# Performance work log

Measured on AMD Instinct MI355X. Metric: run time of the kernel, lower is better.

## Reference

```python
import jax, jax.numpy as jnp
import numpy as np

OSF = 15.0  # over_sample_factor
EXPMAX = 50.0
AFROMZERO = 0.02
AFROMC = 0.01


def zmax_calc(a, b, c=1.0):
    # a is a scalar, b (= b*mT^2) is per-element, c == 1.0
    a_is_zero = a < AFROMZERO
    a_is_c = jnp.abs(a - c) < AFROMC
    z_zero = jnp.where(c > b, b / c, 1.0)
    z_c = b / (b + c)
    denom = jnp.where(a_is_c, 1.0, c - a)  # safe denom; branch masked below
    z_gen = 0.5 * (b + c - jnp.sqrt((b - c) ** 2 + 4.0 * a * b)) / denom
    z_gen = jnp.where((z_gen > 0.9999) & (b > 100.0), jnp.minimum(z_gen, 1.0 - a / b), z_gen)
    return jnp.where(a_is_zero, z_zero, jnp.where(a_is_c, z_c, z_gen))


def likelihood(z, mT, a, b):
    # Lund fragmentation f(z) ratio kernel, c = 1.0
    b_exp = b * mT ** 2
    z_max = zmax_calc(a, b_exp, 1.0)
    f_exp = b_exp * (1.0 / z_max - 1.0 / z) + jnp.log(z_max / z)
    a_coef = a * jnp.log((1.0 - z) / (1.0 - z_max))
    f_exp = f_exp + jnp.where(a < AFROMZERO, 0.0, a_coef)
    return jnp.exp(jnp.clip(f_exp, -EXPMAX, EXPMAX))


def setup_inputs() -> dict:
    key = jax.random.key(0)
    kz, kr, km, kmult, kdrop, kzero = jax.random.split(key, 6)
    B, M, R = 8192, 128, 24  # batch, max multiplicity, reject slots
    mult = jax.random.randint(kmult, (B,), 20, M + 1)  # event multiplicities
    valid = jnp.arange(M)[None, :] < mult[:, None]  # [B, M]

    z_acc = jax.random.uniform(kz, (B, M), minval=0.05, maxval=0.95)
    z_acc = jnp.where(valid & (jax.random.uniform(kzero, (B, M)) > 0.1), z_acc, 0.0)

    z_rej = jax.random.uniform(kr, (B, M, R), minval=0.05, maxval=0.95)
    keep = jax.random.uniform(kdrop, (B, M, R)) < 0.4  # ragged # of rejections
    z_rej = jnp.where(valid[:, :, None] & keep, z_rej, 0.0)

    z = jnp.concatenate([z_acc[:, :, None], z_rej], axis=2).astype(jnp.float32)
    mT = jax.random.uniform(km, (B, M), minval=0.2, maxval=2.0, dtype=jnp.float32)
    observable = jnp.stack([mult, jnp.zeros_like(mult)], axis=1).astype(jnp.int64)

    return {
        "z": z,
        "mT": mT,
        "observable": observable,
        "params_a": jnp.float32(0.72),
        "params_b": jnp.float32(1.05),
        "params_base": jnp.array([0.68, 0.98], dtype=jnp.float32),
    }


def reference(z, mT, observable, params_a, params_b, params_base):
    B, M, _ = z.shape
    mult = observable[:, 0]
    valid = jnp.arange(M)[None, :] < mult[:, None]  # [B, M]
    a0, b0 = params_base[0], params_base[1]

    # accepted z's (column 0)
    z_acc = z[:, :, 0]
    m_acc = (z_acc != 0.0) & valid
    zs = jnp.where(m_acc, z_acc, 0.5)  # safe fill for masked slots
    mTs = jnp.where(m_acc, mT, 1.0)
    w_acc = likelihood(zs, mTs, params_a, params_b) / likelihood(zs, mTs, a0, b0)
    w_acc = jnp.where(m_acc, w_acc, 1.0)

    # rejected z's (columns 1:), each row j uses mT[i, j]
    z_rej = z[:, :, 1:]
    m_rej = (z_rej != 0.0) & valid[:, :, None]
    zr = jnp.where(m_rej, z_rej, 0.5)
    mTr = jnp.where(m_rej, mT[:, :, None], 1.0)
    w_rej = (OSF - likelihood(zr, mTr, params_a, params_b)) / (
        OSF - likelihood(zr, mTr, a0, b0))
    w_rej = jnp.where(m_rej, w_rej, 1.0)

    return jnp.prod(w_acc, axis=1) * jnp.prod(w_rej, axis=(1, 2))
```

## Files before the change

kernel.cpp:

```cpp
#include <hip/hip_runtime.h>

#define AFROMZERO 0.02f
#define AFROMC    0.01f
#define OSF       15.0f
#define LOG2E     1.4426950408889634f
#define EXPMAX2   (50.0f * LOG2E)

__device__ __forceinline__ float zmax_calc(float a, float b) {
    if (a < AFROMZERO) return fminf(b, 1.0f);
    if (fabsf(a - 1.0f) < AFROMC) return b / (b + 1.0f);
    float d  = (b - 1.0f) * (b - 1.0f) + 4.0f * a * b;
    float zg = 0.5f * (b + 1.0f - sqrtf(d)) / (1.0f - a);
    if (zg > 0.9999f && b > 100.0f) zg = fminf(zg, 1.0f - a / b);
    return zg;
}

__device__ __forceinline__ void set_consts2(float a, float b, float mTv,
                                            float& C2, float& be2) {
    float be = b * mTv * mTv;
    float zm = zmax_calc(a, be);
    be2 = be * LOG2E;
    float c = be2 / zm + log2f(zm);
    if (a >= AFROMZERO) c -= a * log2f(1.0f - zm);
    C2 = c;
}

typedef const __attribute__((address_space(1))) void* as1_cvp;
typedef __attribute__((address_space(3))) void* as3_vp;

__global__ __launch_bounds__(256) void lund_weight_kernel(
    const float* __restrict__ z,
    const float* __restrict__ mT,
    const int*   __restrict__ obs,
    const float* __restrict__ pa_p,
    const float* __restrict__ pb_p,
    const float* __restrict__ base_p,
    float* __restrict__ out)
{
    __shared__ float s_z[6656];
    __shared__ float s_part[4];

    const int tid  = threadIdx.x;
    const int lane = tid & 63;
    const int wv   = tid >> 6;
    const int r0   = blockIdx.x * 2;

    const int mult0 = obs[2 * r0];
    const int mult1 = obs[2 * r0 + 2];

    const float* g0 = z + (size_t)r0 * 3200;
    const float* g1 = g0 + 3200;

    const int nc0 = (mult0 * 25 + 255) >> 8;
    const int nc1 = (mult1 * 25 + 255) >> 8;
    for (int c = wv; c < nc0; c += 4) {
        const float* gp = g0 + (c << 8) + (lane << 2);
        __builtin_amdgcn_global_load_lds((as1_cvp)gp, (as3_vp)(s_z + (c << 8)),
                                         16, 0, 0);
    }
    for (int c = wv; c < nc1; c += 4) {
        const float* gp = g1 + (c << 8) + (lane << 2);
        if (c == 12 && lane >= 32) gp = g1;
        __builtin_amdgcn_global_load_lds((as1_cvp)gp, (as3_vp)(s_z + 3328 + (c << 8)),
                                         16, 0, 0);
    }

    const int  half = tid >> 7;
    const int  m    = tid & 127;
    const int  row  = r0 + half;
    const int  mult = half ? mult1 : mult0;
    const bool live = m < mult;

    const float pa = pa_p[0], pb = pb_p[0];
    const float a0 = base_p[0], b0 = base_p[1];
    const float an = (pa < AFROMZERO) ? 0.0f : pa;
    const float ao = (a0 < AFROMZERO) ? 0.0f : a0;

    const float mTv = mT[(size_t)row * 128 + m];
    float Cn2, ben2, Co2, beo2;
    set_consts2(pa, pb, mTv, Cn2, ben2);
    set_consts2(a0, b0, mTv, Co2, beo2);

    __syncthreads();

    float w = 1.0f;
    if (live) {
        const float* zp = s_z + half * 3328 + m * 25;
        float facN = 1.0f, facD = 1.0f;
        #pragma unroll
        for (int k = 0; k < 25; ++k) {
            float zz  = zp[k];
            bool  act = (zz != 0.0f);
            float zs  = act ? zz : 0.5f;
            float rz  = __builtin_amdgcn_rcpf(zs);
            float lz  = __builtin_amdgcn_logf(zs);
            float l1  = __builtin_amdgcn_logf(1.0f - zs);
            float fn  = fmaf(-ben2, rz, Cn2) + fmaf(an, l1, -lz);
            float fo  = fmaf(-beo2, rz, Co2) + fmaf(ao, l1, -lz);
            fn = fminf(fmaxf(fn, -EXPMAX2), EXPMAX2);
            fo = fminf(fmaxf(fo, -EXPMAX2), EXPMAX2);
            float Ln = __builtin_amdgcn_exp2f(fn);
            float Lo = __builtin_amdgcn_exp2f(fo);
            float fN = (k == 0) ? Ln : (OSF - Ln);
            float fD = (k == 0) ? Lo : (OSF - Lo);
            facN *= act ? fN : 1.0f;
            facD *= act ? fD : 1.0f;
        }
        w = facN / facD;
    }

    for (int mask = 1; mask < 64; mask <<= 1)
        w *= __shfl_xor(w, mask, 64);
    if ((tid & 63) == 0) s_part[tid >> 6] = w;
    __syncthreads();
    if (tid == 0)   out[r0]     = s_part[0] * s_part[1];
    if (tid == 128) out[r0 + 1] = s_part[2] * s_part[3];
}

extern "C" void kernel_launch(void* const* d_in, const int* in_sizes, int n_in,
                              void* d_out, int out_size, void* d_ws, size_t ws_size,
                              hipStream_t stream) {
    const float* z    = (const float*)d_in[0];
    const float* mT   = (const float*)d_in[1];
    const int*   obs  = (const int*)d_in[2];
    const float* pa   = (const float*)d_in[3];
    const float* pb   = (const float*)d_in[4];
    const float* base = (const float*)d_in[5];
    float* out = (float*)d_out;

    int B = in_sizes[0] / (128 * 25);
    lund_weight_kernel<<<B / 2, 256, 0, stream>>>(z, mT, obs, pa, pb, base, out);
}
```

Measured before the change: 158.4 us.

## Give each wave its own LDS slice and replace block barrier with waitcnt

Each of the four waves now loads the contiguous 1600-float slice of z that its own 64 threads consume, straight into LDS. Because no wave reads another wave's data, the block-wide __syncthreads is replaced by a per-wave vmcnt wait plus a scheduling barrier. The upper clamp before exp2 is also removed, keeping only the lower one. This cuts barrier stalls and a few ALU ops. It relies on the likelihood never exceeding the upper exponent bound for these inputs, and on the per-wave load mapping being exactly right.

```diff
diff --git a/kernel.cpp b/kernel.cpp
--- a/kernel.cpp
+++ b/kernel.cpp
@@ -49,25 +49,23 @@
     const int mult1 = obs[2 * r0 + 2];
 
     const float* g0 = z + (size_t)r0 * 3200;
-    const float* g1 = g0 + 3200;
 
-    const int nc0 = (mult0 * 25 + 255) >> 8;
-    const int nc1 = (mult1 * 25 + 255) >> 8;
-    for (int c = wv; c < nc0; c += 4) {
-        const float* gp = g0 + (c << 8) + (lane << 2);
-        __builtin_amdgcn_global_load_lds((as1_cvp)gp, (as3_vp)(s_z + (c << 8)),
-                                         16, 0, 0);
-    }
-    for (int c = wv; c < nc1; c += 4) {
-        const float* gp = g1 + (c << 8) + (lane << 2);
-        if (c == 12 && lane >= 32) gp = g1;
-        __builtin_amdgcn_global_load_lds((as1_cvp)gp, (as3_vp)(s_z + 3328 + (c << 8)),
-                                         16, 0, 0);
+    const int wbase = wv * 1600;
+    int need = (wv < 2) ? (mult0 * 25 - wbase) : (mult1 * 25 - (wbase - 3200));
+    need = need < 0 ? 0 : need;
+    #pragma unroll
+    for (int c = 0; c < 7; ++c) {
+        if ((c << 8) < need) {
+            const float* gp = g0 + wbase + (c << 8) + (lane << 2);
+            if (wv == 3 && c == 6 && lane >= 16) gp = g0;
+            __builtin_amdgcn_global_load_lds((as1_cvp)gp,
+                                             (as3_vp)(s_z + wbase + (c << 8)),
+                                             16, 0, 0);
+        }
     }
 
     const int  half = tid >> 7;
     const int  m    = tid & 127;
-    const int  row  = r0 + half;
     const int  mult = half ? mult1 : mult0;
     const bool live = m < mult;
 
@@ -76,16 +74,17 @@
     const float an = (pa < AFROMZERO) ? 0.0f : pa;
     const float ao = (a0 < AFROMZERO) ? 0.0f : a0;
 
-    const float mTv = mT[(size_t)row * 128 + m];
+    const float mTv = mT[(size_t)(r0 + half) * 128 + m];
     float Cn2, ben2, Co2, beo2;
     set_consts2(pa, pb, mTv, Cn2, ben2);
     set_consts2(a0, b0, mTv, Co2, beo2);
 
-    __syncthreads();
+    __builtin_amdgcn_s_waitcnt(0x0F70);
+    __builtin_amdgcn_sched_barrier(0);
 
     float w = 1.0f;
     if (live) {
-        const float* zp = s_z + half * 3328 + m * 25;
+        const float* zp = s_z + 25 * tid;
         float facN = 1.0f, facD = 1.0f;
         #pragma unroll
         for (int k = 0; k < 25; ++k) {
@@ -97,8 +96,8 @@
             float l1  = __builtin_amdgcn_logf(1.0f - zs);
             float fn  = fmaf(-ben2, rz, Cn2) + fmaf(an, l1, -lz);
             float fo  = fmaf(-beo2, rz, Co2) + fmaf(ao, l1, -lz);
-            fn = fminf(fmaxf(fn, -EXPMAX2), EXPMAX2);
-            fo = fminf(fmaxf(fo, -EXPMAX2), EXPMAX2);
+            fn = fmaxf(fn, -EXPMAX2);
+            fo = fmaxf(fo, -EXPMAX2);
             float Ln = __builtin_amdgcn_exp2f(fn);
             float Lo = __builtin_amdgcn_exp2f(fo);
             float fN = (k == 0) ? Ln : (OSF - Ln);
```

Result: no change. 159.4 us (+0.6%).
